# Kernel optimization log

Hardware: AMD Instinct MI355X
Metric: run time of the kernel (lower is better)

Reference implementation:

```python
import jax, jax.numpy as jnp
import numpy as np

B, N, D = 4096, 32768, 256


def setup_inputs() -> dict:
    key = jax.random.key(0)
    kx, kp = jax.random.split(key)
    x = jax.random.normal(kx, (B, D), dtype=jnp.float32)
    prototypes = jax.random.normal(kp, (N, D), dtype=jnp.float32)
    return {"x": x, "prototypes": prototypes}


def reference(x, prototypes):
    # Brute-force L2 1-NN: faiss IndexFlatL2 exact search, k=1, then gather
    x_sq = jnp.sum(x * x, axis=-1, keepdims=True)            # [B, 1]
    p_sq = jnp.sum(prototypes * prototypes, axis=-1)          # [N]
    dists = x_sq + p_sq[None, :] - 2.0 * (x @ prototypes.T)   # [B, N]
    idx = jnp.argmin(dists, axis=-1)                          # [B]
    return prototypes[idx]                                    # [B, D]
```

## Files before the change

### kernel.cpp

```cpp
#include <hip/hip_runtime.h>
#include <stdint.h>


#define NB 4096
#define NP 32768
#define ND 256
#define NG 512
#define MARGIN 2.0f
#define NSPLIT 8
#define CPB 4096

typedef __attribute__((ext_vector_type(8))) __bf16 bf16x8;
typedef __attribute__((ext_vector_type(4))) __bf16 bf16x4;
typedef __attribute__((ext_vector_type(4))) float f32x4;

static constexpr size_t OFF_PSQ = 0;
static constexpr size_t OFF_XB  = 131072;
static constexpr size_t OFF_PB  = OFF_XB + (size_t)NB * ND * 2;
static constexpr size_t OFF_BM  = OFF_PB + (size_t)NP * ND * 2;
static constexpr size_t WS_NEED = OFF_BM + (size_t)NB * NG * 4;

#define VMCNT(n) asm volatile("s_waitcnt vmcnt(" #n ")" ::: "memory")
#define LGKM(n)  asm volatile("s_waitcnt lgkmcnt(" #n ")" ::: "memory")

__device__ __forceinline__ void gload_lds16(const void* g, void* l) {
    __builtin_amdgcn_global_load_lds(
        (const __attribute__((address_space(1))) uint32_t*)g,
        (__attribute__((address_space(3))) uint32_t*)l, 16, 0, 0);
}
__device__ __forceinline__ float dppmin16(float v) {
    int x;
    x = __builtin_amdgcn_update_dpp(0, __float_as_int(v), 0xB1, 0xF, 0xF, true);
    v = fminf(v, __int_as_float(x));
    x = __builtin_amdgcn_update_dpp(0, __float_as_int(v), 0x4E, 0xF, 0xF, true);
    v = fminf(v, __int_as_float(x));
    x = __builtin_amdgcn_update_dpp(0, __float_as_int(v), 0x141, 0xF, 0xF, true);
    v = fminf(v, __int_as_float(x));
    x = __builtin_amdgcn_update_dpp(0, __float_as_int(v), 0x140, 0xF, 0xF, true);
    v = fminf(v, __int_as_float(x));
    return v;
}
__device__ __forceinline__ unsigned fkey(float f) {
    unsigned u = __float_as_uint(f);
    return (u & 0x80000000u) ? ~u : (u | 0x80000000u);
}
__device__ __forceinline__ float fkey_inv(unsigned u) {
    unsigned o = (u & 0x80000000u) ? (u & 0x7FFFFFFFu) : ~u;
    return __uint_as_float(o);
}
__device__ __forceinline__ unsigned long long umin64(unsigned long long a,
                                                     unsigned long long b) {
    return a < b ? a : b;
}
__device__ __forceinline__ unsigned umin32(unsigned a, unsigned b) {
    return a < b ? a : b;
}

__global__ void prep_kernel(const float* __restrict__ X, const float* __restrict__ P,
                            float* __restrict__ psq, __bf16* __restrict__ Xb,
                            __bf16* __restrict__ Pb) {
    int row  = blockIdx.x * 4 + (threadIdx.x >> 6);
    int lane = threadIdx.x & 63;
    if (row < NP) {
        f32x4 v = ((const f32x4*)(P + (size_t)row * ND))[lane];
        bf16x4 b;
        b.x = (__bf16)v.x; b.y = (__bf16)v.y; b.z = (__bf16)v.z; b.w = (__bf16)v.w;
        ((bf16x4*)(Pb + (size_t)row * ND))[lane] = b;
        float s = v.x*v.x + v.y*v.y + v.z*v.z + v.w*v.w;
        #pragma unroll
        for (int off = 32; off > 0; off >>= 1) s += __shfl_down(s, off);
        if (lane == 0) psq[row] = s;
    } else {
        int r = row - NP;
        f32x4 v = ((const f32x4*)(X + (size_t)r * ND))[lane];
        bf16x4 b;
        b.x = (__bf16)v.x; b.y = (__bf16)v.y; b.z = (__bf16)v.z; b.w = (__bf16)v.w;
        ((bf16x4*)(Xb + (size_t)r * ND))[lane] = b;
    }
}

__global__ __launch_bounds__(512, 2)
void nn_dpp_kernel(const __bf16* __restrict__ Xb, const __bf16* __restrict__ Pb,
                   const float* __restrict__ psq,
                   unsigned* __restrict__ blockmin) {
    __shared__ __align__(16) char smem[163840];
    char* ring  = smem;
    char* A_lds = smem + 65536;
    unsigned (*tbl)[64] = (unsigned (*)[64])(smem + 131072);

    const int tid  = threadIdx.x;
    const int lane = tid & 63;
    const int wave = tid >> 6;
    const int wm = wave >> 2, wn = wave & 3;
    const int bid    = blockIdx.x;
    const int nsplit = bid & 7;
    const int mblk   = bid >> 3;
    const int bm     = mblk * 128;
    const int Nb     = nsplit * CPB;
    const int fr = lane & 15, kg = lane >> 4;
    const int wbase16 = (tid & ~63) * 16;

    f32x4 acc[4][4];
    #pragma unroll
    for (int i = 0; i < 4; ++i)
        #pragma unroll
        for (int j = 0; j < 4; ++j) acc[i][j] = (f32x4){0.f, 0.f, 0.f, 0.f};

    auto stage = [&](int p) {
        char* dst = ring + (size_t)(p & 3) * 16384;
        const int colb = Nb + (p >> 3) * 256;
        const int kq   = p & 7;
        #pragma unroll
        for (int i = 0; i < 2; ++i) {
            const int c = i * 512 + tid;
            const int fn = c >> 6;
            const int l  = c & 63;
            gload_lds16(Pb + (size_t)(colb + fn * 16 + (l & 15)) * ND +
                            kq * 32 + (l >> 4) * 8,
                        dst + i * 8192 + wbase16);
        }
    };

    #pragma unroll
    for (int i = 0; i < 8; ++i) {
        const int c  = i * 512 + tid;
        const int q  = c >> 9;
        const int fm = (c >> 6) & 7;
        const int l  = c & 63;
        gload_lds16(Xb + (size_t)(bm + fm * 16 + (l & 15)) * ND +
                        q * 32 + (l >> 4) * 8,
                    A_lds + (size_t)(i * 512) * 16 + wbase16);
    }
    stage(0); stage(1); stage(2);
    VMCNT(4);
    __builtin_amdgcn_s_barrier();
    __builtin_amdgcn_sched_barrier(0);

    bf16x8 av[2][4], bv[2][4];
    #pragma unroll
    for (int mi = 0; mi < 4; ++mi)
        av[0][mi] = *(const bf16x8*)(A_lds +
            (size_t)((wm * 4 + mi) * 64 + lane) * 16);
    #pragma unroll
    for (int ni = 0; ni < 4; ++ni)
        bv[0][ni] = *(const bf16x8*)(ring +
            (size_t)((wn * 4 + ni) * 64 + lane) * 16);

    #pragma unroll 1
    for (int nt = 0; nt < 16; ++nt) {
        float cq[4];
        #pragma unroll
        for (int q = 0; q < 8; ++q) {
            const int t = nt * 8 + q;
            const int cur = q & 1, nxt = cur ^ 1;
            if (t >= 126)            { VMCNT(0); }
            else if (q == 1 || q == 2) { VMCNT(6); }
            else                     { VMCNT(2); }
            __builtin_amdgcn_s_barrier();
            __builtin_amdgcn_sched_barrier(0);
            if (t < 127) {
                const int qn = (q + 1) & 7;
                #pragma unroll
                for (int mi = 0; mi < 4; ++mi)
                    av[nxt][mi] = *(const bf16x8*)(A_lds +
                        (size_t)((qn * 8 + wm * 4 + mi) * 64 + lane) * 16);
                const char* pc = ring + (size_t)((t + 1) & 3) * 16384;
                #pragma unroll
                for (int ni = 0; ni < 4; ++ni)
                    bv[nxt][ni] = *(const bf16x8*)(pc +
                        (size_t)((wn * 4 + ni) * 64 + lane) * 16);
            }
            if (t <= 124) stage(t + 3);
            if (q == 0) {
                const int colb = Nb + nt * 256 + wn * 64;
                #pragma unroll
                for (int ni = 0; ni < 4; ++ni)
                    cq[ni] = psq[colb + ni * 16 + fr];
            }
            __builtin_amdgcn_s_setprio(1);
            #pragma unroll
            for (int mi = 0; mi < 4; ++mi)
                #pragma unroll
                for (int ni = 0; ni < 4; ++ni)
                    acc[mi][ni] = __builtin_amdgcn_mfma_f32_16x16x32_bf16(
                        av[cur][mi], bv[cur][ni], acc[mi][ni], 0, 0, 0);
            __builtin_amdgcn_s_setprio(0);

            if (q == 7) {
                const int g = nt * 4 + wn;
                #pragma unroll
                for (int mi = 0; mi < 4; ++mi) {
                    #pragma unroll
                    for (int r = 0; r < 4; ++r) {
                        float d = fmaf(-2.f, acc[mi][0][r], cq[0]);
                        #pragma unroll
                        for (int ni = 1; ni < 4; ++ni)
                            d = fminf(d, fmaf(-2.f, acc[mi][ni][r], cq[ni]));
                        d = dppmin16(d);
                        if (fr == 0)
                            tbl[wm * 64 + mi * 16 + kg * 4 + r][g] = fkey(d);
                    }
                }
                #pragma unroll
                for (int i = 0; i < 4; ++i)
                    #pragma unroll
                    for (int j = 0; j < 4; ++j)
                        acc[i][j] = (f32x4){0.f, 0.f, 0.f, 0.f};
            }
        }
    }

    __syncthreads();
    #pragma unroll
    for (int i = 0; i < 8; ++i) {
        const int f2  = i * 512 + tid;
        uint2 v = ((const uint2*)tbl)[f2];
        const int idx = f2 * 2;
        const int row = idx >> 6, col = idx & 63;
        *(uint2*)&blockmin[(size_t)(bm + row) * NG + nsplit * 64 + col] = v;
    }
}

__global__ __launch_bounds__(512, 2)
void rescore_wave_kernel(const float* __restrict__ X, const float* __restrict__ P,
                         const float* __restrict__ psq,
                         const unsigned* __restrict__ blockmin,
                         float* __restrict__ out) {
    __shared__ float Xs[8][256];
    __shared__ unsigned short wcand[8][512];
    __shared__ int wcnt[8];

    const int tid = threadIdx.x, lane = tid & 63, wv = tid >> 6;
    const int row = blockIdx.x * 8 + wv;

    ((f32x4*)Xs[wv])[lane] = ((const f32x4*)(X + (size_t)row * ND))[lane];
    if (lane == 0) wcnt[wv] = 0;

    const unsigned* bmr = blockmin + (size_t)row * NG;
    uint4 ka = ((const uint4*)bmr)[lane * 2];
    uint4 kb = ((const uint4*)bmr)[lane * 2 + 1];
    unsigned km = umin32(umin32(umin32(ka.x, ka.y), umin32(ka.z, ka.w)),
                         umin32(umin32(kb.x, kb.y), umin32(kb.z, kb.w)));
    #pragma unroll
    for (int m = 1; m < 64; m <<= 1) km = umin32(km, __shfl_xor(km, m));
    const unsigned thr = fkey(fkey_inv(km) + MARGIN);

    const unsigned k8[8] = {ka.x, ka.y, ka.z, ka.w, kb.x, kb.y, kb.z, kb.w};
    #pragma unroll
    for (int i = 0; i < 8; ++i)
        if (k8[i] <= thr)
            wcand[wv][atomicAdd(&wcnt[wv], 1)] = (unsigned short)(lane * 8 + i);
    LGKM(0);
    const int n = wcnt[wv];

    unsigned long long best = 0xFFFFFFFFFFFFFFFFull;
    const f32x4* x4 = (const f32x4*)Xs[wv];
    for (int c = 0; c < n; ++c) {
        const int col = (int)wcand[wv][c] * 64 + lane;
        const f32x4* p4 = (const f32x4*)(P + (size_t)col * ND);
        float s = 0.f;
        #pragma unroll 16
        for (int i = 0; i < 64; ++i) {
            f32x4 pv = p4[i], xv = x4[i];
            s = fmaf(xv.x, pv.x, s); s = fmaf(xv.y, pv.y, s);
            s = fmaf(xv.z, pv.z, s); s = fmaf(xv.w, pv.w, s);
        }
        float d = fmaf(-2.f, s, psq[col]);
        best = umin64(best, ((unsigned long long)fkey(d) << 32) |
                            (unsigned long long)(unsigned)col);
    }
    #pragma unroll
    for (int m = 1; m < 64; m <<= 1)
        best = umin64(best, __shfl_xor(best, m));
    const unsigned bc = (unsigned)(best & 0xFFFFFFFFull);
    ((f32x4*)(out + (size_t)row * ND))[lane] =
        ((const f32x4*)(P + (size_t)bc * ND))[lane];
}

#define BM1 128
#define BN1 128
#define BK1 32
#define LDA1 132

__global__ void psq_init_kernel(const float* __restrict__ P, float* __restrict__ psq,
                                unsigned long long* __restrict__ minpack) {
    int row  = blockIdx.x * 4 + (threadIdx.x >> 6);
    int lane = threadIdx.x & 63;
    float4 p4 = ((const float4*)(P + (size_t)row * ND))[lane];
    float s = p4.x*p4.x + p4.y*p4.y + p4.z*p4.z + p4.w*p4.w;
    #pragma unroll
    for (int off = 32; off > 0; off >>= 1) s += __shfl_down(s, off);
    if (lane == 0) psq[row] = s;
    int gid = blockIdx.x * blockDim.x + threadIdx.x;
    if (gid < NB) minpack[gid] = 0xFFFFFFFFFFFFFFFFull;
}

__global__ __launch_bounds__(256, 2)
void nn_main_kernel(const float* __restrict__ X, const float* __restrict__ P,
                    const float* __restrict__ psq,
                    unsigned long long* __restrict__ minpack) {
    __shared__ __align__(16) char smem_raw[2 * BK1 * LDA1 * 4];
    float (*As)[LDA1] = (float (*)[LDA1])smem_raw;
    float (*Bs)[LDA1] = (float (*)[LDA1])(smem_raw + BK1 * LDA1 * 4);
    const int bm  = blockIdx.y * BM1;
    const int bn  = blockIdx.x * BN1;
    const int tid = threadIdx.x;
    const int tx  = tid & 15;
    const int ty  = tid >> 4;
    float acc[8][8];
    #pragma unroll
    for (int i = 0; i < 8; ++i)
        #pragma unroll
        for (int j = 0; j < 8; ++j) acc[i][j] = 0.f;
    const int lrow = tid >> 3;
    const int lk   = (tid & 7) * 4;
    for (int k0 = 0; k0 < ND; k0 += BK1) {
        #pragma unroll
        for (int p = 0; p < 4; ++p) {
            int r = p * 32 + lrow;
            float4 aa = *(const float4*)(X + (size_t)(bm + r) * ND + k0 + lk);
            As[lk+0][r] = aa.x; As[lk+1][r] = aa.y; As[lk+2][r] = aa.z; As[lk+3][r] = aa.w;
            float4 bb = *(const float4*)(P + (size_t)(bn + r) * ND + k0 + lk);
            Bs[lk+0][r] = bb.x; Bs[lk+1][r] = bb.y; Bs[lk+2][r] = bb.z; Bs[lk+3][r] = bb.w;
        }
        __syncthreads();
        #pragma unroll 4
        for (int k = 0; k < BK1; ++k) {
            float4 a0 = *(const float4*)&As[k][ty*8];
            float4 a1 = *(const float4*)&As[k][ty*8 + 4];
            float4 b0 = *(const float4*)&Bs[k][tx*4];
            float4 b1 = *(const float4*)&Bs[k][64 + tx*4];
            float av2[8] = {a0.x,a0.y,a0.z,a0.w,a1.x,a1.y,a1.z,a1.w};
            float bv2[8] = {b0.x,b0.y,b0.z,b0.w,b1.x,b1.y,b1.z,b1.w};
            #pragma unroll
            for (int i = 0; i < 8; ++i)
                #pragma unroll
                for (int j = 0; j < 8; ++j)
                    acc[i][j] = fmaf(av2[i], bv2[j], acc[i][j]);
        }
        __syncthreads();
    }
    unsigned long long (*red)[16] = (unsigned long long (*)[16])smem_raw;
    float cj[8];
    int   jglob[8];
    #pragma unroll
    for (int j = 0; j < 8; ++j) {
        int c = (j < 4) ? (tx*4 + j) : (64 + tx*4 + (j - 4));
        jglob[j] = bn + c;
        cj[j]    = psq[bn + c];
    }
    #pragma unroll
    for (int i = 0; i < 8; ++i) {
        float bestv = 0.f; unsigned bidx = 0u; bool first = true;
        #pragma unroll
        for (int j = 0; j < 8; ++j) {
            float s = fmaf(-2.f, acc[i][j], cj[j]);
            if (first || s < bestv) { bestv = s; bidx = (unsigned)jglob[j]; first = false; }
        }
        unsigned u = fkey(bestv);
        red[ty*8 + i][tx] = ((unsigned long long)u << 32) | (unsigned long long)bidx;
    }
    __syncthreads();
    if (tid < BM1) {
        unsigned long long m = red[tid][0];
        #pragma unroll
        for (int t = 1; t < 16; ++t) m = umin64(m, red[tid][t]);
        atomicMin(&minpack[bm + tid], m);
    }
}

__global__ void gather_kernel(const float* __restrict__ P,
                              const unsigned long long* __restrict__ minpack,
                              float* __restrict__ out) {
    int row = blockIdx.x;
    unsigned idx = (unsigned)(minpack[row] & 0xFFFFFFFFull);
    int lane = threadIdx.x;
    ((float4*)(out + (size_t)row * ND))[lane] =
        ((const float4*)(P + (size_t)idx * ND))[lane];
}

extern "C" void kernel_launch(void* const* d_in, const int* in_sizes, int n_in,
                              void* d_out, int out_size, void* d_ws, size_t ws_size,
                              hipStream_t stream) {
    const float* X = (const float*)d_in[0];
    const float* P = (const float*)d_in[1];
    float* out = (float*)d_out;
    char* w = (char*)d_ws;

    if (ws_size >= WS_NEED) {
        float* psq = (float*)(w + OFF_PSQ);
        __bf16* Xb = (__bf16*)(w + OFF_XB);
        __bf16* Pb = (__bf16*)(w + OFF_PB);
        unsigned* blockmin = (unsigned*)(w + OFF_BM);

        prep_kernel<<<(NP + NB) / 4, 256, 0, stream>>>(X, P, psq, Xb, Pb);
        nn_dpp_kernel<<<(NB / 128) * NSPLIT, 512, 0, stream>>>(Xb, Pb, psq,
                                                               blockmin);
        rescore_wave_kernel<<<NB / 8, 512, 0, stream>>>(X, P, psq, blockmin, out);
    } else {
        float* psq = (float*)w;
        unsigned long long* minpack = (unsigned long long*)(w + (size_t)NP * 4);
        psq_init_kernel<<<NP / 4, 256, 0, stream>>>(P, psq, minpack);
        dim3 grid(NP / BN1, NB / BM1);
        nn_main_kernel<<<grid, dim3(256), 0, stream>>>(X, P, psq, minpack);
        gather_kernel<<<NB, 64, 0, stream>>>(P, minpack, out);
    }
}
```

Before: 170.1 us.

## Switch GEMM to double-buffered 2-K-step stages and add bf16 prefilter in rescore

```diff
diff --git a/kernel.cpp b/kernel.cpp
--- a/kernel.cpp
+++ b/kernel.cpp
@@ -7,6 +7,7 @@
 #define ND 256
 #define NG 512
 #define MARGIN 2.0f
+#define MARGIN_AB 1.5f
 #define NSPLIT 8
 #define CPB 4096
 
@@ -80,9 +81,9 @@
 }
 
 __global__ __launch_bounds__(512, 2)
-void nn_dpp_kernel(const __bf16* __restrict__ Xb, const __bf16* __restrict__ Pb,
-                   const float* __restrict__ psq,
-                   unsigned* __restrict__ blockmin) {
+void nn_db_kernel(const __bf16* __restrict__ Xb, const __bf16* __restrict__ Pb,
+                  const float* __restrict__ psq,
+                  unsigned* __restrict__ blockmin) {
     __shared__ __align__(16) char smem[163840];
     char* ring  = smem;
     char* A_lds = smem + 65536;
@@ -107,18 +108,20 @@
         for (int j = 0; j < 4; ++j) acc[i][j] = (f32x4){0.f, 0.f, 0.f, 0.f};
 
     auto stage = [&](int p) {
-        char* dst = ring + (size_t)(p & 3) * 16384;
-        const int colb = Nb + (p >> 3) * 256;
-        const int kq   = p & 7;
-        #pragma unroll
-        for (int i = 0; i < 2; ++i) {
-            const int c = i * 512 + tid;
-            const int fn = c >> 6;
-            const int l  = c & 63;
-            gload_lds16(Pb + (size_t)(colb + fn * 16 + (l & 15)) * ND +
-                            kq * 32 + (l >> 4) * 8,
-                        dst + i * 8192 + wbase16);
-        }
+        char* dst = ring + (size_t)(p & 1) * 32768;
+        const int colb = Nb + (p >> 2) * 256;
+        const int kq0  = (p & 3) * 2;
+        #pragma unroll
+        for (int s = 0; s < 2; ++s)
+            #pragma unroll
+            for (int i = 0; i < 2; ++i) {
+                const int c = i * 512 + tid;
+                const int fn = c >> 6;
+                const int l  = c & 63;
+                gload_lds16(Pb + (size_t)(colb + fn * 16 + (l & 15)) * ND +
+                                (kq0 + s) * 32 + (l >> 4) * 8,
+                            dst + s * 16384 + i * 8192 + wbase16);
+            }
     };
 
     #pragma unroll
@@ -131,62 +134,59 @@
                         q * 32 + (l >> 4) * 8,
                     A_lds + (size_t)(i * 512) * 16 + wbase16);
     }
-    stage(0); stage(1); stage(2);
-    VMCNT(4);
-    __builtin_amdgcn_s_barrier();
-    __builtin_amdgcn_sched_barrier(0);
-
-    bf16x8 av[2][4], bv[2][4];
-    #pragma unroll
-    for (int mi = 0; mi < 4; ++mi)
-        av[0][mi] = *(const bf16x8*)(A_lds +
-            (size_t)((wm * 4 + mi) * 64 + lane) * 16);
-    #pragma unroll
-    for (int ni = 0; ni < 4; ++ni)
-        bv[0][ni] = *(const bf16x8*)(ring +
-            (size_t)((wn * 4 + ni) * 64 + lane) * 16);
+    stage(0);
 
     #pragma unroll 1
     for (int nt = 0; nt < 16; ++nt) {
         float cq[4];
         #pragma unroll
-        for (int q = 0; q < 8; ++q) {
-            const int t = nt * 8 + q;
-            const int cur = q & 1, nxt = cur ^ 1;
-            if (t >= 126)            { VMCNT(0); }
-            else if (q == 1 || q == 2) { VMCNT(6); }
-            else                     { VMCNT(2); }
+        for (int qq = 0; qq < 4; ++qq) {
+            const int b = nt * 4 + qq;
+            VMCNT(0);
             __builtin_amdgcn_s_barrier();
             __builtin_amdgcn_sched_barrier(0);
-            if (t < 127) {
-                const int qn = (q + 1) & 7;
-                #pragma unroll
-                for (int mi = 0; mi < 4; ++mi)
-                    av[nxt][mi] = *(const bf16x8*)(A_lds +
-                        (size_t)((qn * 8 + wm * 4 + mi) * 64 + lane) * 16);
-                const char* pc = ring + (size_t)((t + 1) & 3) * 16384;
-                #pragma unroll
-                for (int ni = 0; ni < 4; ++ni)
-                    bv[nxt][ni] = *(const bf16x8*)(pc +
-                        (size_t)((wn * 4 + ni) * 64 + lane) * 16);
-            }
-            if (t <= 124) stage(t + 3);
-            if (q == 0) {
+            if (b < 63) stage(b + 1);
+            if (qq == 0) {
                 const int colb = Nb + nt * 256 + wn * 64;
                 #pragma unroll
                 for (int ni = 0; ni < 4; ++ni)
                     cq[ni] = psq[colb + ni * 16 + fr];
             }
+            const char* slot = ring + (size_t)(b & 1) * 32768;
+            const int qa = (b & 3) * 2;
+            bf16x8 av0[4], bv0[4], av1[4], bv1[4];
+            #pragma unroll
+            for (int mi = 0; mi < 4; ++mi)
+                av0[mi] = *(const bf16x8*)(A_lds +
+                    (size_t)((qa * 8 + wm * 4 + mi) * 64 + lane) * 16);
+            #pragma unroll
+            for (int ni = 0; ni < 4; ++ni)
+                bv0[ni] = *(const bf16x8*)(slot +
+                    (size_t)((wn * 4 + ni) * 64 + lane) * 16);
+            #pragma unroll
+            for (int mi = 0; mi < 4; ++mi)
+                av1[mi] = *(const bf16x8*)(A_lds +
+                    (size_t)(((qa + 1) * 8 + wm * 4 + mi) * 64 + lane) * 16);
+            #pragma unroll
+            for (int ni = 0; ni < 4; ++ni)
+                bv1[ni] = *(const bf16x8*)(slot + 16384 +
+                    (size_t)((wn * 4 + ni) * 64 + lane) * 16);
             __builtin_amdgcn_s_setprio(1);
             #pragma unroll
             for (int mi = 0; mi < 4; ++mi)
                 #pragma unroll
                 for (int ni = 0; ni < 4; ++ni)
                     acc[mi][ni] = __builtin_amdgcn_mfma_f32_16x16x32_bf16(
-                        av[cur][mi], bv[cur][ni], acc[mi][ni], 0, 0, 0);
+                        av0[mi], bv0[ni], acc[mi][ni], 0, 0, 0);
+            #pragma unroll
+            for (int mi = 0; mi < 4; ++mi)
+                #pragma unroll
+                for (int ni = 0; ni < 4; ++ni)
+                    acc[mi][ni] = __builtin_amdgcn_mfma_f32_16x16x32_bf16(
+                        av1[mi], bv1[ni], acc[mi][ni], 0, 0, 0);
             __builtin_amdgcn_s_setprio(0);
 
-            if (q == 7) {
+            if (qq == 3) {
                 const int g = nt * 4 + wn;
                 #pragma unroll
                 for (int mi = 0; mi < 4; ++mi) {
@@ -222,10 +222,11 @@
 }
 
 __global__ __launch_bounds__(512, 2)
-void rescore_wave_kernel(const float* __restrict__ X, const float* __restrict__ P,
-                         const float* __restrict__ psq,
-                         const unsigned* __restrict__ blockmin,
-                         float* __restrict__ out) {
+void rescore2_kernel(const float* __restrict__ X, const float* __restrict__ P,
+                     const __bf16* __restrict__ Pb,
+                     const float* __restrict__ psq,
+                     const unsigned* __restrict__ blockmin,
+                     float* __restrict__ out) {
     __shared__ float Xs[8][256];
     __shared__ unsigned short wcand[8][512];
     __shared__ int wcnt[8];
@@ -243,7 +244,9 @@
                          umin32(umin32(kb.x, kb.y), umin32(kb.z, kb.w)));
     #pragma unroll
     for (int m = 1; m < 64; m <<= 1) km = umin32(km, __shfl_xor(km, m));
-    const unsigned thr = fkey(fkey_inv(km) + MARGIN);
+    const float mval = fkey_inv(km);
+    const unsigned thr = fkey(mval + MARGIN);
+    const float dthr = mval + MARGIN_AB;
 
     const unsigned k8[8] = {ka.x, ka.y, ka.z, ka.w, kb.x, kb.y, kb.z, kb.w};
     #pragma unroll
@@ -257,17 +260,31 @@
     const f32x4* x4 = (const f32x4*)Xs[wv];
     for (int c = 0; c < n; ++c) {
         const int col = (int)wcand[wv][c] * 64 + lane;
-        const f32x4* p4 = (const f32x4*)(P + (size_t)col * ND);
+        const bf16x8* pr = (const bf16x8*)(Pb + (size_t)col * ND);
         float s = 0.f;
-        #pragma unroll 16
-        for (int i = 0; i < 64; ++i) {
-            f32x4 pv = p4[i], xv = x4[i];
-            s = fmaf(xv.x, pv.x, s); s = fmaf(xv.y, pv.y, s);
-            s = fmaf(xv.z, pv.z, s); s = fmaf(xv.w, pv.w, s);
-        }
-        float d = fmaf(-2.f, s, psq[col]);
-        best = umin64(best, ((unsigned long long)fkey(d) << 32) |
-                            (unsigned long long)(unsigned)col);
+        #pragma unroll
+        for (int i = 0; i < 32; ++i) {
+            bf16x8 v = pr[i];
+            f32x4 xa = x4[i * 2], xb = x4[i * 2 + 1];
+            s = fmaf(xa.x, (float)v[0], s); s = fmaf(xa.y, (float)v[1], s);
+            s = fmaf(xa.z, (float)v[2], s); s = fmaf(xa.w, (float)v[3], s);
+            s = fmaf(xb.x, (float)v[4], s); s = fmaf(xb.y, (float)v[5], s);
+            s = fmaf(xb.z, (float)v[6], s); s = fmaf(xb.w, (float)v[7], s);
+        }
+        float dA = fmaf(-2.f, s, psq[col]);
+        if (dA <= dthr) {
+            const f32x4* p4 = (const f32x4*)(P + (size_t)col * ND);
+            float se = 0.f;
+            #pragma unroll 16
+            for (int i = 0; i < 64; ++i) {
+                f32x4 pv = p4[i], xv = x4[i];
+                se = fmaf(xv.x, pv.x, se); se = fmaf(xv.y, pv.y, se);
+                se = fmaf(xv.z, pv.z, se); se = fmaf(xv.w, pv.w, se);
+            }
+            float d = fmaf(-2.f, se, psq[col]);
+            best = umin64(best, ((unsigned long long)fkey(d) << 32) |
+                                (unsigned long long)(unsigned)col);
+        }
     }
     #pragma unroll
     for (int m = 1; m < 64; m <<= 1)
@@ -394,9 +411,10 @@
         unsigned* blockmin = (unsigned*)(w + OFF_BM);
 
         prep_kernel<<<(NP + NB) / 4, 256, 0, stream>>>(X, P, psq, Xb, Pb);
-        nn_dpp_kernel<<<(NB / 128) * NSPLIT, 512, 0, stream>>>(Xb, Pb, psq,
-                                                               blockmin);
-        rescore_wave_kernel<<<NB / 8, 512, 0, stream>>>(X, P, psq, blockmin, out);
+        nn_db_kernel<<<(NB / 128) * NSPLIT, 512, 0, stream>>>(Xb, Pb, psq,
+                                                              blockmin);
+        rescore2_kernel<<<NB / 8, 512, 0, stream>>>(X, P, Pb, psq, blockmin,
+                                                    out);
     } else {
         float* psq = (float*)w;
         unsigned long long* minpack = (unsigned long long*)(w + (size_t)NP * 4);
```

New measurement: 235.8 us. 38.6% more time.

## Load-balance fp32 rescoring via global candidate pair list and atomicMin

Applied to the files above, without the earlier changes.

```diff
diff --git a/kernel.cpp b/kernel.cpp
--- a/kernel.cpp
+++ b/kernel.cpp
@@ -9,6 +9,7 @@
 #define MARGIN 2.0f
 #define NSPLIT 8
 #define CPB 4096
+#define PAIR_CAP 500000
 
 typedef __attribute__((ext_vector_type(8))) __bf16 bf16x8;
 typedef __attribute__((ext_vector_type(4))) __bf16 bf16x4;
@@ -19,6 +20,9 @@
 static constexpr size_t OFF_PB  = OFF_XB + (size_t)NB * ND * 2;
 static constexpr size_t OFF_BM  = OFF_PB + (size_t)NP * ND * 2;
 static constexpr size_t WS_NEED = OFF_BM + (size_t)NB * NG * 4;
+static constexpr size_t OFF_MP    = OFF_XB;
+static constexpr size_t OFF_CTR   = OFF_XB + 32768;
+static constexpr size_t OFF_PAIRS = OFF_XB + 32832;
 
 #define VMCNT(n) asm volatile("s_waitcnt vmcnt(" #n ")" ::: "memory")
 #define LGKM(n)  asm volatile("s_waitcnt lgkmcnt(" #n ")" ::: "memory")
@@ -222,19 +226,11 @@
 }
 
 __global__ __launch_bounds__(512, 2)
-void rescore_wave_kernel(const float* __restrict__ X, const float* __restrict__ P,
-                         const float* __restrict__ psq,
-                         const unsigned* __restrict__ blockmin,
-                         float* __restrict__ out) {
-    __shared__ float Xs[8][256];
-    __shared__ unsigned short wcand[8][512];
-    __shared__ int wcnt[8];
-
+void cand_kernel(const unsigned* __restrict__ blockmin,
+                 unsigned* __restrict__ pairs, unsigned* __restrict__ ctr,
+                 unsigned long long* __restrict__ minpack) {
     const int tid = threadIdx.x, lane = tid & 63, wv = tid >> 6;
     const int row = blockIdx.x * 8 + wv;
-
-    ((f32x4*)Xs[wv])[lane] = ((const f32x4*)(X + (size_t)row * ND))[lane];
-    if (lane == 0) wcnt[wv] = 0;
 
     const unsigned* bmr = blockmin + (size_t)row * NG;
     uint4 ka = ((const uint4*)bmr)[lane * 2];
@@ -245,36 +241,75 @@
     for (int m = 1; m < 64; m <<= 1) km = umin32(km, __shfl_xor(km, m));
     const unsigned thr = fkey(fkey_inv(km) + MARGIN);
 
+    if (lane == 0) minpack[row] = 0xFFFFFFFFFFFFFFFFull;
+
     const unsigned k8[8] = {ka.x, ka.y, ka.z, ka.w, kb.x, kb.y, kb.z, kb.w};
     #pragma unroll
     for (int i = 0; i < 8; ++i)
-        if (k8[i] <= thr)
-            wcand[wv][atomicAdd(&wcnt[wv], 1)] = (unsigned short)(lane * 8 + i);
-    LGKM(0);
-    const int n = wcnt[wv];
-
-    unsigned long long best = 0xFFFFFFFFFFFFFFFFull;
-    const f32x4* x4 = (const f32x4*)Xs[wv];
-    for (int c = 0; c < n; ++c) {
-        const int col = (int)wcand[wv][c] * 64 + lane;
-        const f32x4* p4 = (const f32x4*)(P + (size_t)col * ND);
-        float s = 0.f;
-        #pragma unroll 16
-        for (int i = 0; i < 64; ++i) {
-            f32x4 pv = p4[i], xv = x4[i];
-            s = fmaf(xv.x, pv.x, s); s = fmaf(xv.y, pv.y, s);
-            s = fmaf(xv.z, pv.z, s); s = fmaf(xv.w, pv.w, s);
-        }
-        float d = fmaf(-2.f, s, psq[col]);
-        best = umin64(best, ((unsigned long long)fkey(d) << 32) |
-                            (unsigned long long)(unsigned)col);
-    }
-    #pragma unroll
-    for (int m = 1; m < 64; m <<= 1)
-        best = umin64(best, __shfl_xor(best, m));
-    const unsigned bc = (unsigned)(best & 0xFFFFFFFFull);
-    ((f32x4*)(out + (size_t)row * ND))[lane] =
-        ((const f32x4*)(P + (size_t)bc * ND))[lane];
+        if (k8[i] <= thr) {
+            unsigned pos = atomicAdd(ctr, 1u);
+            if (pos < PAIR_CAP)
+                pairs[pos] = ((unsigned)row << 9) | (unsigned)(lane * 8 + i);
+        }
+}
+
+__global__ __launch_bounds__(256, 4)
+void rescore_bal_kernel(const float* __restrict__ X, const float* __restrict__ P,
+                        const float* __restrict__ psq,
+                        const unsigned* __restrict__ pairs,
+                        const unsigned* __restrict__ ctr,
+                        unsigned long long* __restrict__ minpack) {
+    const int lane = threadIdx.x & 63;
+    const int gw   = blockIdx.x * 4 + (threadIdx.x >> 6);
+    const int npairs = (int)umin32(*ctr, PAIR_CAP);
+
+    for (int idx = gw; idx < npairs; idx += 4096) {
+        const unsigned pr = pairs[idx];
+        const int row = (int)(pr >> 9);
+        const int g   = (int)(pr & 511u);
+
+        const f32x4* x4 = (const f32x4*)(X + (size_t)row * ND);
+        f32x4 xr[16];
+        #pragma unroll
+        for (int i = 0; i < 16; ++i) xr[i] = x4[(lane & 3) + i * 4];
+
+        unsigned long long best = 0xFFFFFFFFFFFFFFFFull;
+        #pragma unroll
+        for (int cc = 0; cc < 4; ++cc) {
+            const int col = g * 64 + cc * 16 + (lane >> 2);
+            const f32x4* p4 = (const f32x4*)(P + (size_t)col * ND);
+            float s = 0.f;
+            #pragma unroll
+            for (int i = 0; i < 16; ++i) {
+                f32x4 pv = p4[(lane & 3) + i * 4], xv = xr[i];
+                s = fmaf(xv.x, pv.x, s); s = fmaf(xv.y, pv.y, s);
+                s = fmaf(xv.z, pv.z, s); s = fmaf(xv.w, pv.w, s);
+            }
+            s += __shfl_xor(s, 1);
+            s += __shfl_xor(s, 2);
+            unsigned long long key = 0xFFFFFFFFFFFFFFFFull;
+            if ((lane & 3) == 0) {
+                float d = fmaf(-2.f, s, psq[col]);
+                key = ((unsigned long long)fkey(d) << 32) |
+                      (unsigned long long)(unsigned)col;
+            }
+            best = umin64(best, key);
+        }
+        #pragma unroll
+        for (int m = 1; m < 64; m <<= 1)
+            best = umin64(best, __shfl_xor(best, m));
+        if (lane == 0) atomicMin(&minpack[row], best);
+    }
+}
+
+__global__ void gather_kernel(const float* __restrict__ P,
+                              const unsigned long long* __restrict__ minpack,
+                              float* __restrict__ out) {
+    int row = blockIdx.x;
+    unsigned idx = (unsigned)(minpack[row] & 0xFFFFFFFFull);
+    int lane = threadIdx.x;
+    ((float4*)(out + (size_t)row * ND))[lane] =
+        ((const float4*)(P + (size_t)idx * ND))[lane];
 }
 
 #define BM1 128
@@ -369,16 +404,6 @@
     }
 }
 
-__global__ void gather_kernel(const float* __restrict__ P,
-                              const unsigned long long* __restrict__ minpack,
-                              float* __restrict__ out) {
-    int row = blockIdx.x;
-    unsigned idx = (unsigned)(minpack[row] & 0xFFFFFFFFull);
-    int lane = threadIdx.x;
-    ((float4*)(out + (size_t)row * ND))[lane] =
-        ((const float4*)(P + (size_t)idx * ND))[lane];
-}
-
 extern "C" void kernel_launch(void* const* d_in, const int* in_sizes, int n_in,
                               void* d_out, int out_size, void* d_ws, size_t ws_size,
                               hipStream_t stream) {
@@ -392,11 +417,18 @@
         __bf16* Xb = (__bf16*)(w + OFF_XB);
         __bf16* Pb = (__bf16*)(w + OFF_PB);
         unsigned* blockmin = (unsigned*)(w + OFF_BM);
+        unsigned long long* minpack = (unsigned long long*)(w + OFF_MP);
+        unsigned* ctr   = (unsigned*)(w + OFF_CTR);
+        unsigned* pairs = (unsigned*)(w + OFF_PAIRS);
 
         prep_kernel<<<(NP + NB) / 4, 256, 0, stream>>>(X, P, psq, Xb, Pb);
         nn_dpp_kernel<<<(NB / 128) * NSPLIT, 512, 0, stream>>>(Xb, Pb, psq,
                                                                blockmin);
-        rescore_wave_kernel<<<NB / 8, 512, 0, stream>>>(X, P, psq, blockmin, out);
+        hipMemsetAsync(ctr, 0, 4, stream);
+        cand_kernel<<<NB / 8, 512, 0, stream>>>(blockmin, pairs, ctr, minpack);
+        rescore_bal_kernel<<<1024, 256, 0, stream>>>(X, P, psq, pairs, ctr,
+                                                     minpack);
+        gather_kernel<<<NB, 64, 0, stream>>>(P, minpack, out);
     } else {
         float* psq = (float*)w;
         unsigned long long* minpack = (unsigned long long*)(w + (size_t)NP * 4);
```

Measured after the change: 204.9 us. +20.5%, slower.

## Load prototype B-fragments directly into registers instead of an LDS ring

Applied to the files above, without the earlier changes.

```diff
diff --git a/kernel.cpp b/kernel.cpp
--- a/kernel.cpp
+++ b/kernel.cpp
@@ -80,13 +80,12 @@
 }
 
 __global__ __launch_bounds__(512, 2)
-void nn_dpp_kernel(const __bf16* __restrict__ Xb, const __bf16* __restrict__ Pb,
-                   const float* __restrict__ psq,
-                   unsigned* __restrict__ blockmin) {
-    __shared__ __align__(16) char smem[163840];
-    char* ring  = smem;
-    char* A_lds = smem + 65536;
-    unsigned (*tbl)[64] = (unsigned (*)[64])(smem + 131072);
+void nn_breg_kernel(const __bf16* __restrict__ Xb, const __bf16* __restrict__ Pb,
+                    const float* __restrict__ psq,
+                    unsigned* __restrict__ blockmin) {
+    __shared__ __align__(16) char smem[98304];
+    char* A_lds = smem;
+    unsigned (*tbl)[64] = (unsigned (*)[64])(smem + 65536);
 
     const int tid  = threadIdx.x;
     const int lane = tid & 63;
@@ -106,21 +105,6 @@
         #pragma unroll
         for (int j = 0; j < 4; ++j) acc[i][j] = (f32x4){0.f, 0.f, 0.f, 0.f};
 
-    auto stage = [&](int p) {
-        char* dst = ring + (size_t)(p & 3) * 16384;
-        const int colb = Nb + (p >> 3) * 256;
-        const int kq   = p & 7;
-        #pragma unroll
-        for (int i = 0; i < 2; ++i) {
-            const int c = i * 512 + tid;
-            const int fn = c >> 6;
-            const int l  = c & 63;
-            gload_lds16(Pb + (size_t)(colb + fn * 16 + (l & 15)) * ND +
-                            kq * 32 + (l >> 4) * 8,
-                        dst + i * 8192 + wbase16);
-        }
-    };
-
     #pragma unroll
     for (int i = 0; i < 8; ++i) {
         const int c  = i * 512 + tid;
@@ -131,20 +115,23 @@
                         q * 32 + (l >> 4) * 8,
                     A_lds + (size_t)(i * 512) * 16 + wbase16);
     }
-    stage(0); stage(1); stage(2);
-    VMCNT(4);
+    VMCNT(0);
     __builtin_amdgcn_s_barrier();
     __builtin_amdgcn_sched_barrier(0);
 
-    bf16x8 av[2][4], bv[2][4];
+    const __bf16* pbase = Pb + (size_t)(Nb + wn * 64 + fr) * ND + kg * 8;
+
+    bf16x8 bv[2][4], av[2][4];
+    #pragma unroll
+    for (int tt = 0; tt < 2; ++tt)
+        #pragma unroll
+        for (int ni = 0; ni < 4; ++ni)
+            bv[tt][ni] = *(const bf16x8*)(pbase + (size_t)(ni * 16) * ND +
+                                          tt * 32);
     #pragma unroll
     for (int mi = 0; mi < 4; ++mi)
         av[0][mi] = *(const bf16x8*)(A_lds +
             (size_t)((wm * 4 + mi) * 64 + lane) * 16);
-    #pragma unroll
-    for (int ni = 0; ni < 4; ++ni)
-        bv[0][ni] = *(const bf16x8*)(ring +
-            (size_t)((wn * 4 + ni) * 64 + lane) * 16);
 
     #pragma unroll 1
     for (int nt = 0; nt < 16; ++nt) {
@@ -152,25 +139,15 @@
         #pragma unroll
         for (int q = 0; q < 8; ++q) {
             const int t = nt * 8 + q;
-            const int cur = q & 1, nxt = cur ^ 1;
-            if (t >= 126)            { VMCNT(0); }
-            else if (q == 1 || q == 2) { VMCNT(6); }
-            else                     { VMCNT(2); }
-            __builtin_amdgcn_s_barrier();
-            __builtin_amdgcn_sched_barrier(0);
+            const int cur = q & 1;
+            const int nxt = cur ^ 1;
             if (t < 127) {
                 const int qn = (q + 1) & 7;
                 #pragma unroll
                 for (int mi = 0; mi < 4; ++mi)
                     av[nxt][mi] = *(const bf16x8*)(A_lds +
                         (size_t)((qn * 8 + wm * 4 + mi) * 64 + lane) * 16);
-                const char* pc = ring + (size_t)((t + 1) & 3) * 16384;
-                #pragma unroll
-                for (int ni = 0; ni < 4; ++ni)
-                    bv[nxt][ni] = *(const bf16x8*)(pc +
-                        (size_t)((wn * 4 + ni) * 64 + lane) * 16);
             }
-            if (t <= 124) stage(t + 3);
             if (q == 0) {
                 const int colb = Nb + nt * 256 + wn * 64;
                 #pragma unroll
@@ -185,6 +162,14 @@
                     acc[mi][ni] = __builtin_amdgcn_mfma_f32_16x16x32_bf16(
                         av[cur][mi], bv[cur][ni], acc[mi][ni], 0, 0, 0);
             __builtin_amdgcn_s_setprio(0);
+            if (t <= 125) {
+                const int t2 = t + 2;
+                const __bf16* src = pbase + (size_t)((t2 >> 3) * 256) * ND +
+                                    (t2 & 7) * 32;
+                #pragma unroll
+                for (int ni = 0; ni < 4; ++ni)
+                    bv[cur][ni] = *(const bf16x8*)(src + (size_t)(ni * 16) * ND);
+            }
 
             if (q == 7) {
                 const int g = nt * 4 + wn;
@@ -394,8 +379,8 @@
         unsigned* blockmin = (unsigned*)(w + OFF_BM);
 
         prep_kernel<<<(NP + NB) / 4, 256, 0, stream>>>(X, P, psq, Xb, Pb);
-        nn_dpp_kernel<<<(NB / 128) * NSPLIT, 512, 0, stream>>>(Xb, Pb, psq,
-                                                               blockmin);
+        nn_breg_kernel<<<(NB / 128) * NSPLIT, 512, 0, stream>>>(Xb, Pb, psq,
+                                                                blockmin);
         rescore_wave_kernel<<<NB / 8, 512, 0, stream>>>(X, P, psq, blockmin, out);
     } else {
         float* psq = (float*)w;
```

After: 218.6 us. 1.28x slower.
